# Performance work log

Measured on AMD Instinct MI355X. Metric: run time of the kernel, lower is better.

## Reference

```python
import jax, jax.numpy as jnp
import numpy as np

NEG_INF = -1e30
NUM_HEADS = 4
MEM_LEN = 16
RECURRENT_STEPS = 3
B, PLEN, GLEN, D = 16, 512, 16384, 256


def gated_attn(query, key, value, key_mask, Wq, Wk, Wv, Wo, Wg, bg):
    # GatedMultiHeadAttn.forward (pre/post lnorm off, add_zero_attn off, eval dropout)
    b, qlen, _ = query.shape
    klen = key.shape[1]
    hidden = Wq.shape[1]
    hd = hidden // NUM_HEADS
    hq = (query @ Wq).reshape(b, qlen, NUM_HEADS, hd)
    hk = (key @ Wk).reshape(b, klen, NUM_HEADS, hd)
    hv = (value @ Wv).reshape(b, klen, NUM_HEADS, hd)
    scale = 1.0 / np.sqrt(hd).astype(np.float32)
    score = jnp.einsum('bind,bjnd->bijn', hq, hk) * scale
    score = jnp.where((key_mask == 0)[:, None, :, None], NEG_INF, score)
    attn = jax.nn.softmax(score, axis=2)  # normalize over keys j
    vec = jnp.einsum('bijn,bjnd->bind', attn, hv).reshape(b, qlen, hidden)
    attn_out = vec @ Wo
    gate = jax.nn.sigmoid(jnp.concatenate([query, attn_out], axis=-1) @ Wg + bg)
    return gate * query + (1.0 - gate) * attn_out


def _attn_params(key, query_dim, kv_dim, hidden):
    ks = jax.random.split(key, 6)
    scale = 1.0 / np.sqrt(hidden // NUM_HEADS)
    Wq = jax.random.normal(ks[0], (query_dim, hidden), jnp.float32) * scale
    Wk = jax.random.normal(ks[1], (kv_dim, hidden), jnp.float32) * scale
    Wv = jax.random.normal(ks[2], (kv_dim, hidden), jnp.float32) * scale
    Wo = jax.random.normal(ks[3], (hidden, query_dim), jnp.float32) * scale
    Wg = jax.random.normal(ks[4], (2 * query_dim, query_dim), jnp.float32) * scale
    bg = jnp.ones((query_dim,), jnp.float32)
    return Wq, Wk, Wv, Wo, Wg, bg


def setup_inputs() -> dict:
    key = jax.random.key(0)
    ks = jax.random.split(key, 4)
    inp = {
        'pattern': jax.random.normal(ks[0], (B, PLEN, D), jnp.float32),
        'graph': jax.random.normal(ks[1], (B, GLEN, D), jnp.float32),
        'pattern_mask': jnp.ones((B, PLEN), jnp.int32),
        'graph_mask': jnp.ones((B, GLEN), jnp.int32),
    }
    p = _attn_params(ks[2], D, D, D)
    g = _attn_params(ks[3], D, D, D)
    for n, v in zip(['p_Wq', 'p_Wk', 'p_Wv', 'p_Wo', 'p_Wg', 'p_bg'], p):
        inp[n] = v
    for n, v in zip(['g_Wq', 'g_Wk', 'g_Wv', 'g_Wo', 'g_Wg', 'g_bg'], g):
        inp[n] = v
    return inp


def reference(pattern, graph, pattern_mask, graph_mask,
              p_Wq, p_Wk, p_Wv, p_Wo, p_Wg, p_bg,
              g_Wq, g_Wk, g_Wv, g_Wo, g_Wg, g_bg):
    b, glen, d = graph.shape
    stride = glen // MEM_LEN
    kernel = glen - (MEM_LEN - 1) * stride
    assert stride == kernel  # mem_len divides glen -> avg_pool1d == segment mean
    mem = graph.reshape(b, MEM_LEN, kernel, d).mean(axis=2)  # init_mem 'mean'
    mem_mask = graph_mask.reshape(b, MEM_LEN, kernel).max(axis=2)
    for _ in range(RECURRENT_STEPS):
        mem = gated_attn(mem, pattern, pattern, pattern_mask,
                         p_Wq, p_Wk, p_Wv, p_Wo, p_Wg, p_bg)
        mem = gated_attn(mem, graph, graph, graph_mask,
                         g_Wq, g_Wk, g_Wv, g_Wo, g_Wg, g_bg)
    return mem
```

## Files before the change

kernel.cpp:

```cpp
#include <hip/hip_runtime.h>
#include <stdint.h>

#define NH 4
#define HD 64
#define DM 256
#define BB 16
#define PLEN 512
#define GLEN 16384
#define ML 16
#define NCH_MAX 32

typedef __attribute__((ext_vector_type(8))) short bf16x8;
typedef __attribute__((ext_vector_type(4))) short s16x4;
typedef __attribute__((ext_vector_type(4))) float f32x4;
struct fl4 { float x, y, z, w; };

#define MFMA16(a, b, c) __builtin_amdgcn_mfma_f32_16x16x32_bf16((a), (b), (c), 0, 0, 0)

__device__ __forceinline__ float bf2f(short x) {
  union { unsigned u; float f; } v;
  v.u = ((unsigned)(unsigned short)x) << 16;
  return v.f;
}
__device__ __forceinline__ short f2bf(float x) {
  union { float f; unsigned u; } v;
  v.f = x;
  unsigned u = v.u;
  u += 0x7fffu + ((u >> 16) & 1u);
  return (short)(u >> 16);
}

__global__ void detect_dtype(const short* __restrict__ pattern, int* __restrict__ flag) {
  int t = threadIdx.x;
  int bad = 0;
  for (int i = t; i < 4096; i += 256) {
    float v = bf2f(pattern[2 * i]);
    if (!(fabsf(v) < 1e10f)) bad++;
  }
  __shared__ int cnt;
  if (t == 0) cnt = 0;
  __syncthreads();
  if (bad) atomicAdd(&cnt, bad);
  __syncthreads();
  if (t == 0) flag[0] = (cnt > 8) ? 1 : 0;
}

__global__ __launch_bounds__(256) void convert_sum(
    const void* __restrict__ src, short* __restrict__ dst,
    float* __restrict__ partials, const int* __restrict__ flag, int do_sum) {
  int isf = flag[0];
  int t = threadIdx.x;
  int r4 = t >> 6, c4 = (t & 63) * 4;
  size_t row0 = (size_t)blockIdx.x * 128;
  float s0 = 0.f, s1 = 0.f, s2 = 0.f, s3 = 0.f;
  if (isf) {
    const float* sf = (const float*)src;
    for (int it = 0; it < 32; it++) {
      size_t row = row0 + it * 4 + r4;
      fl4 v = *(const fl4*)(sf + row * DM + c4);
      s0 += v.x; s1 += v.y; s2 += v.z; s3 += v.w;
      s16x4 o;
      o[0] = f2bf(v.x); o[1] = f2bf(v.y); o[2] = f2bf(v.z); o[3] = f2bf(v.w);
      *(s16x4*)(dst + row * DM + c4) = o;
    }
  } else {
    const short* sb = (const short*)src;
    for (int it = 0; it < 32; it++) {
      size_t row = row0 + it * 4 + r4;
      s16x4 v = *(const s16x4*)(sb + row * DM + c4);
      s0 += bf2f(v[0]); s1 += bf2f(v[1]); s2 += bf2f(v[2]); s3 += bf2f(v[3]);
      *(s16x4*)(dst + row * DM + c4) = v;
    }
  }
  if (!do_sum) return;
  __shared__ float part[4][256];
  part[r4][c4] = s0;
  part[r4][c4 + 1] = s1;
  part[r4][c4 + 2] = s2;
  part[r4][c4 + 3] = s3;
  __syncthreads();
  partials[(size_t)blockIdx.x * 256 + t] =
      part[0][t] + part[1][t] + part[2][t] + part[3][t];
}

__global__ __launch_bounds__(256) void finalize_q0(
    const float* __restrict__ partials, const void* __restrict__ Wq,
    float* __restrict__ mem, short* __restrict__ hq, const int* __restrict__ flag) {
  int b = blockIdx.x >> 4, m = blockIdx.x & 15;
  int t = threadIdx.x;
  int isf = flag[0];
  int p0 = b * 128 + m * 8;
  float s = 0.f;
#pragma unroll
  for (int i = 0; i < 8; i++) s += partials[(size_t)(p0 + i) * 256 + t];
  float v = s * (1.0f / 1024.0f);
  __shared__ float memrow[256];
  memrow[t] = bf2f(f2bf(v));
  mem[((size_t)b * ML + m) * DM + t] = v;
  __syncthreads();
  float acc = 0.f;
  if (isf) {
    const float* wf = (const float*)Wq;
    for (int k = 0; k < 256; k++)
      acc += memrow[k] * bf2f(f2bf(wf[(size_t)k * 256 + t]));
  } else {
    const short* wsp = (const short*)Wq;
    for (int k = 0; k < 256; k++)
      acc += memrow[k] * bf2f(wsp[(size_t)k * 256 + t]);
  }
  hq[((size_t)b * ML + m) * DM + t] = f2bf(acc);
}

struct WTArgs {
  const void* src[10];
  short* dst[10];
  int rows[10];
};

__global__ void transpose_w(WTArgs a, const int* __restrict__ flag) {
  int mid = blockIdx.z;
  int K = a.rows[mid];
  int tk = blockIdx.x, tn = blockIdx.y;
  if (tk * 32 >= K) return;
  int isf = flag[0];
  __shared__ short tile[32][33];
  const short* src = (const short*)a.src[mid];
  const float* srcf = (const float*)a.src[mid];
  short* dst = a.dst[mid];
  int tx = threadIdx.x, ty = threadIdx.y;
  for (int i = 0; i < 32; i += 8) {
    size_t idx = (size_t)(tk * 32 + ty + i) * 256 + tn * 32 + tx;
    tile[ty + i][tx] = isf ? f2bf(srcf[idx]) : src[idx];
  }
  __syncthreads();
  for (int i = 0; i < 32; i += 8)
    dst[(size_t)(tn * 32 + ty + i) * K + tk * 32 + tx] = tile[tx][ty + i];
}

__global__ void conv_bias(const void* p_bg, const void* g_bg, short* out,
                          const int* __restrict__ flag) {
  int t = threadIdx.x;
  int isf = flag[0];
  out[t] = isf ? f2bf(((const float*)p_bg)[t]) : ((const short*)p_bg)[t];
  out[256 + t] = isf ? f2bf(((const float*)g_bg)[t]) : ((const short*)g_bg)[t];
}

__global__ __launch_bounds__(512, 2) void proj_kv(
    const short* __restrict__ X, const short* __restrict__ WkT,
    const short* __restrict__ WvT, short* __restrict__ Kout,
    short* __restrict__ Vt, int L) {
  __shared__ __align__(16) short Xs[128 * 32];
  __shared__ __align__(16) short Ws[256 * 32];
  const short* WT = blockIdx.y ? WvT : WkT;
  int row0 = blockIdx.x * 128;
  int t = threadIdx.x;
  int wave = t >> 6, lane = t & 63, quad = lane >> 4, l16 = lane & 15;
  int wrow = (wave >> 2) * 64, wcol = (wave & 3) * 64;
  int tr = t >> 2, tc = t & 3;
  f32x4 z = {0.f, 0.f, 0.f, 0.f};
  f32x4 acc[4][4];
#pragma unroll
  for (int i = 0; i < 4; i++)
#pragma unroll
    for (int j = 0; j < 4; j++) acc[i][j] = z;

  for (int kk = 0; kk < 8; kk++) {
    bf16x8 x0 = *(const bf16x8*)(X + (size_t)(row0 + tr) * DM + kk * 32 + tc * 8);
    bf16x8 w0 = *(const bf16x8*)(WT + (size_t)tr * DM + kk * 32 + tc * 8);
    bf16x8 w1 = *(const bf16x8*)(WT + (size_t)(tr + 128) * DM + kk * 32 + tc * 8);
    *(bf16x8*)(Xs + tr * 32 + tc * 8) = x0;
    *(bf16x8*)(Ws + tr * 32 + tc * 8) = w0;
    *(bf16x8*)(Ws + (tr + 128) * 32 + tc * 8) = w1;
    __syncthreads();
    bf16x8 af[4], bfr[4];
#pragma unroll
    for (int rt = 0; rt < 4; rt++)
      af[rt] = *(const bf16x8*)(Xs + (wrow + rt * 16 + l16) * 32 + quad * 8);
#pragma unroll
    for (int ct = 0; ct < 4; ct++)
      bfr[ct] = *(const bf16x8*)(Ws + (wcol + ct * 16 + l16) * 32 + quad * 8);
#pragma unroll
    for (int rt = 0; rt < 4; rt++)
#pragma unroll
      for (int ct = 0; ct < 4; ct++)
        acc[rt][ct] = MFMA16(af[rt], bfr[ct], acc[rt][ct]);
    __syncthreads();
  }
  if (blockIdx.y == 0) {
#pragma unroll
    for (int rt = 0; rt < 4; rt++)
#pragma unroll
      for (int ct = 0; ct < 4; ct++) {
        int col = wcol + ct * 16 + l16;
#pragma unroll
        for (int r = 0; r < 4; r++) {
          int row = row0 + wrow + rt * 16 + quad * 4 + r;
          Kout[(size_t)row * DM + col] = f2bf(acc[rt][ct][r]);
        }
      }
  } else {
#pragma unroll
    for (int rt = 0; rt < 4; rt++) {
      int gr = row0 + wrow + rt * 16 + quad * 4;
      int bb = gr / L, j = gr % L;
#pragma unroll
      for (int ct = 0; ct < 4; ct++) {
        int c = wcol + ct * 16 + l16;
        s16x4 pv;
#pragma unroll
        for (int r = 0; r < 4; r++) pv[r] = f2bf(acc[rt][ct][r]);
        *(s16x4*)(Vt + ((size_t)bb * DM + c) * L + j) = pv;
      }
    }
  }
}

__global__ __launch_bounds__(256, 4) void flash_partial(
    const short* __restrict__ hq, const short* __restrict__ Kb,
    const short* __restrict__ Vt, const int* __restrict__ mask,
    float* __restrict__ pm, float* __restrict__ pl, float* __restrict__ pO,
    int L, int NCH) {
  int ch = blockIdx.x, b = blockIdx.y;
  int C = L / NCH;
  int t = threadIdx.x, wave = t >> 6, lane = t & 63, quad = lane >> 4, l16 = lane & 15;
  __shared__ __align__(16) short Plds[4][512];
  short* myP = &Plds[wave][0];
  const short* qbase = hq + ((size_t)b * ML + l16) * DM + wave * HD;
  bf16x8 aq0 = *(const bf16x8*)(qbase + quad * 8);
  bf16x8 aq1 = *(const bf16x8*)(qbase + 32 + quad * 8);
  f32x4 z = {0.f, 0.f, 0.f, 0.f};
  float m_run[4], l_run[4];
  f32x4 O[4];
#pragma unroll
  for (int r = 0; r < 4; r++) { m_run[r] = -1e30f; l_run[r] = 0.f; }
#pragma unroll
  for (int d = 0; d < 4; d++) O[d] = z;
  int j0 = ch * C;
  const float L2E = 1.44269504f;
  for (int jt = 0; jt < C; jt += 32) {
    f32x4 S[2];
#pragma unroll
    for (int tt = 0; tt < 2; tt++) {
      int j = j0 + jt + tt * 16 + l16;
      const short* kb = Kb + ((size_t)b * L + j) * DM + wave * HD;
      bf16x8 b0 = *(const bf16x8*)(kb + quad * 8);
      bf16x8 b1 = *(const bf16x8*)(kb + 32 + quad * 8);
      f32x4 s = MFMA16(aq0, b0, z);
      s = MFMA16(aq1, b1, s);
      int mk = mask[(size_t)b * L + j];
#pragma unroll
      for (int r = 0; r < 4; r++)
        S[tt][r] = mk ? s[r] * 0.125f : -1e30f;
    }
    float p[2][4], alpha[4];
#pragma unroll
    for (int r = 0; r < 4; r++) {
      float v = fmaxf(S[0][r], S[1][r]);
      v = fmaxf(v, __shfl_xor(v, 1, 16));
      v = fmaxf(v, __shfl_xor(v, 2, 16));
      v = fmaxf(v, __shfl_xor(v, 4, 16));
      v = fmaxf(v, __shfl_xor(v, 8, 16));
      float nm = fmaxf(m_run[r], v);
      alpha[r] = exp2f((m_run[r] - nm) * L2E);
      m_run[r] = nm;
      p[0][r] = exp2f((S[0][r] - nm) * L2E);
      p[1][r] = exp2f((S[1][r] - nm) * L2E);
      float ps = p[0][r] + p[1][r];
      ps += __shfl_xor(ps, 1, 16);
      ps += __shfl_xor(ps, 2, 16);
      ps += __shfl_xor(ps, 4, 16);
      ps += __shfl_xor(ps, 8, 16);
      l_run[r] = l_run[r] * alpha[r] + ps;
    }
#pragma unroll
    for (int d = 0; d < 4; d++)
#pragma unroll
      for (int r = 0; r < 4; r++) O[d][r] *= alpha[r];
#pragma unroll
    for (int tt = 0; tt < 2; tt++)
#pragma unroll
      for (int r = 0; r < 4; r++)
        myP[(quad * 4 + r) * 32 + tt * 16 + l16] = f2bf(p[tt][r]);
    __syncthreads();
    bf16x8 ap = *(const bf16x8*)(myP + l16 * 32 + quad * 8);
#pragma unroll
    for (int d = 0; d < 4; d++) {
      const short* vb = Vt + ((size_t)b * DM + wave * HD + d * 16 + l16) * L + j0 + jt + quad * 8;
      bf16x8 bv = *(const bf16x8*)vb;
      O[d] = MFMA16(ap, bv, O[d]);
    }
    __syncthreads();
  }
  size_t base = (((size_t)b * NCH + ch) * NH + wave) * ML;
  if (l16 == 0) {
#pragma unroll
    for (int r = 0; r < 4; r++) {
      pm[base + quad * 4 + r] = m_run[r];
      pl[base + quad * 4 + r] = l_run[r];
    }
  }
#pragma unroll
  for (int d = 0; d < 4; d++)
#pragma unroll
    for (int r = 0; r < 4; r++)
      pO[(base + quad * 4 + r) * 64 + d * 16 + l16] = O[d][r];
}

__global__ __launch_bounds__(256, 2) void epilogue(
    const float* __restrict__ pm, const float* __restrict__ pl,
    const float* __restrict__ pO, int NCH,
    float* __restrict__ mem, const short* __restrict__ WoT,
    const short* __restrict__ WgT, const short* __restrict__ bg,
    const short* __restrict__ WqT, short* __restrict__ hq,
    void* __restrict__ outb, const int* __restrict__ flag) {
  int b = blockIdx.x, t = threadIdx.x;
  int isf = flag[0];
  __shared__ float w_lds[NCH_MAX * 64];
  __shared__ float invL[64];
  __shared__ __align__(16) short vec_bf[ML * DM];
  __shared__ __align__(16) short mem_bf[ML * DM];
  __shared__ __align__(16) short attn_bf[ML * DM];
  __shared__ float attn_f[ML * DM];
  __shared__ __align__(16) short memn_bf[ML * DM];

  for (int idx = t; idx < ML * DM; idx += 256)
    mem_bf[idx] = f2bf(mem[(size_t)b * ML * DM + idx]);
  if (t < 64) {
    size_t base = (size_t)b * NCH * NH * ML + t;
    float M = -1e30f;
    for (int ch = 0; ch < NCH; ch++)
      M = fmaxf(M, pm[base + (size_t)ch * NH * ML]);
    float Ls = 0.f;
    for (int ch = 0; ch < NCH; ch++) {
      float w = exp2f((pm[base + (size_t)ch * NH * ML] - M) * 1.44269504f);
      w_lds[ch * 64 + t] = w;
      Ls += w * pl[base + (size_t)ch * NH * ML];
    }
    invL[t] = 1.0f / Ls;
  }
  __syncthreads();
  {
    int n = t >> 6, d = t & 63;
    for (int i = 0; i < 16; i++) {
      size_t pb = ((size_t)b * NCH * NH * ML + n * ML + i) * 64 + d;
      float o = 0.f;
      for (int ch = 0; ch < NCH; ch++)
        o += w_lds[ch * 64 + n * 16 + i] * pO[pb + (size_t)ch * NH * ML * 64];
      vec_bf[i * DM + n * 64 + d] = f2bf(o * invL[n * 16 + i]);
    }
  }
  __syncthreads();
  int wave = t >> 6, lane = t & 63, quad = lane >> 4, l16 = lane & 15;
  f32x4 z = {0.f, 0.f, 0.f, 0.f};
  f32x4 acc[4];
#pragma unroll
  for (int c = 0; c < 4; c++) acc[c] = z;
#pragma unroll
  for (int kk = 0; kk < 8; kk++) {
    bf16x8 a = *(const bf16x8*)(vec_bf + l16 * DM + kk * 32 + quad * 8);
#pragma unroll
    for (int ct = 0; ct < 4; ct++) {
      const short* wb = WoT + (size_t)(wave * 64 + ct * 16 + l16) * DM + kk * 32 + quad * 8;
      acc[ct] = MFMA16(a, *(const bf16x8*)wb, acc[ct]);
    }
  }
#pragma unroll
  for (int ct = 0; ct < 4; ct++)
#pragma unroll
    for (int r = 0; r < 4; r++) {
      int row = quad * 4 + r, col = wave * 64 + ct * 16 + l16;
      attn_f[row * DM + col] = acc[ct][r];
      attn_bf[row * DM + col] = f2bf(acc[ct][r]);
    }
  __syncthreads();
  f32x4 g[4];
#pragma unroll
  for (int c = 0; c < 4; c++) g[c] = z;
#pragma unroll
  for (int kk = 0; kk < 16; kk++) {
    bf16x8 a = (kk < 8)
        ? *(const bf16x8*)(mem_bf + l16 * DM + kk * 32 + quad * 8)
        : *(const bf16x8*)(attn_bf + l16 * DM + (kk - 8) * 32 + quad * 8);
#pragma unroll
    for (int ct = 0; ct < 4; ct++) {
      const short* wb = WgT + (size_t)(wave * 64 + ct * 16 + l16) * 512 + kk * 32 + quad * 8;
      g[ct] = MFMA16(a, *(const bf16x8*)wb, g[ct]);
    }
  }
#pragma unroll
  for (int ct = 0; ct < 4; ct++)
#pragma unroll
    for (int r = 0; r < 4; r++) {
      int row = quad * 4 + r, col = wave * 64 + ct * 16 + l16;
      float x = g[ct][r] + bf2f(bg[col]);
      float gg = 1.0f / (1.0f + exp2f(-x * 1.44269504f));
      float old = mem[(size_t)b * ML * DM + row * DM + col];
      float mn = gg * old + (1.0f - gg) * attn_f[row * DM + col];
      mem[(size_t)b * ML * DM + row * DM + col] = mn;
      memn_bf[row * DM + col] = f2bf(mn);
      if (outb) {
        size_t oi = (size_t)b * ML * DM + row * DM + col;
        if (isf) ((float*)outb)[oi] = mn;
        else ((short*)outb)[oi] = f2bf(mn);
      }
    }
  __syncthreads();
  if (WqT) {
    f32x4 h[4];
#pragma unroll
    for (int c = 0; c < 4; c++) h[c] = z;
#pragma unroll
    for (int kk = 0; kk < 8; kk++) {
      bf16x8 a = *(const bf16x8*)(memn_bf + l16 * DM + kk * 32 + quad * 8);
#pragma unroll
      for (int ct = 0; ct < 4; ct++) {
        const short* wb = WqT + (size_t)(wave * 64 + ct * 16 + l16) * DM + kk * 32 + quad * 8;
        h[ct] = MFMA16(a, *(const bf16x8*)wb, h[ct]);
      }
    }
#pragma unroll
    for (int ct = 0; ct < 4; ct++)
#pragma unroll
      for (int r = 0; r < 4; r++)
        hq[(size_t)b * ML * DM + (quad * 4 + r) * DM + wave * 64 + ct * 16 + l16] = f2bf(h[ct][r]);
  }
}

extern "C" void kernel_launch(void* const* d_in, const int* in_sizes, int n_in,
                              void* d_out, int out_size, void* d_ws, size_t ws_size,
                              hipStream_t stream) {
  const void* pattern = d_in[0];
  const void* graph = d_in[1];
  const int* pmask = (const int*)d_in[2];
  const int* gmask = (const int*)d_in[3];

  char* ws = (char*)d_ws;
  size_t off = 0;
  auto alloc = [&](size_t bytes) {
    void* p = ws + off;
    off = (off + bytes + 255) & ~(size_t)255;
    return p;
  };
  int* flag = (int*)alloc(4);
  int rows[10] = {256, 256, 256, 256, 512, 256, 256, 256, 256, 512};
  int srcidx[10] = {4, 5, 6, 7, 8, 10, 11, 12, 13, 14};
  short* WT[10];
  for (int i = 0; i < 10; i++) WT[i] = (short*)alloc((size_t)rows[i] * 256 * 2);
  short* bgc = (short*)alloc(512 * 2);
  short* Kp = (short*)alloc((size_t)BB * PLEN * DM * 2);
  short* Vpt = (short*)alloc((size_t)BB * PLEN * DM * 2);
  short* Kg = (short*)alloc((size_t)BB * GLEN * DM * 2);
  short* Vgt = (short*)alloc((size_t)BB * GLEN * DM * 2);
  short* hq = (short*)alloc((size_t)BB * ML * DM * 2);
  float* memf = (float*)alloc((size_t)BB * ML * DM * 4);
  float* pm = (float*)alloc((size_t)BB * NCH_MAX * NH * ML * 4);
  float* pl = (float*)alloc((size_t)BB * NCH_MAX * NH * ML * 4);
  float* pO = (float*)alloc((size_t)BB * NCH_MAX * NH * ML * 64 * 4);
  float* partG = (float*)alloc((size_t)(BB * GLEN / 128) * 256 * 4);
  short* gbf = (short*)alloc((size_t)BB * GLEN * DM * 2);
  short* pbf = (short*)alloc((size_t)BB * PLEN * DM * 2);
  if (off > ws_size) return;

  detect_dtype<<<dim3(1), dim3(256), 0, stream>>>((const short*)pattern, flag);

  WTArgs wa;
  for (int i = 0; i < 10; i++) {
    wa.src[i] = d_in[srcidx[i]];
    wa.dst[i] = WT[i];
    wa.rows[i] = rows[i];
  }
  transpose_w<<<dim3(16, 8, 10), dim3(32, 8), 0, stream>>>(wa, flag);
  conv_bias<<<dim3(1), dim3(256), 0, stream>>>(d_in[9], d_in[15], bgc, flag);

  convert_sum<<<dim3(BB * GLEN / 128), dim3(256), 0, stream>>>(graph, gbf, partG, flag, 1);
  convert_sum<<<dim3(BB * PLEN / 128), dim3(256), 0, stream>>>(pattern, pbf, (float*)nullptr, flag, 0);
  finalize_q0<<<dim3(BB * ML), dim3(256), 0, stream>>>(partG, d_in[4], memf, hq, flag);

  proj_kv<<<dim3(BB * PLEN / 128, 2), dim3(512), 0, stream>>>(pbf, WT[1], WT[2], Kp, Vpt, PLEN);
  proj_kv<<<dim3(BB * GLEN / 128, 2), dim3(512), 0, stream>>>(gbf, WT[6], WT[7], Kg, Vgt, GLEN);

  for (int s = 0; s < 3; s++) {
    flash_partial<<<dim3(8, BB), dim3(256), 0, stream>>>(hq, Kp, Vpt, pmask, pm, pl, pO, PLEN, 8);
    epilogue<<<dim3(BB), dim3(256), 0, stream>>>(pm, pl, pO, 8, memf, WT[3], WT[4], bgc,
                                                 (const short*)WT[5], hq, (void*)nullptr, flag);
    bool last = (s == 2);
    flash_partial<<<dim3(32, BB), dim3(256), 0, stream>>>(hq, Kg, Vgt, gmask, pm, pl, pO, GLEN, 32);
    epilogue<<<dim3(BB), dim3(256), 0, stream>>>(pm, pl, pO, 32, memf, WT[8], WT[9], bgc + 256,
                                                 last ? (const short*)nullptr : (const short*)WT[0],
                                                 hq, last ? d_out : (void*)nullptr, flag);
  }
}
```

Baseline: 1.195 ms.

## Fuse input conversion and segment sums into K/V projection kernel

Replaces the separate convert_sum pass (fp32→bf16 copy plus column sums) and the two-pass proj_kv with one kernel. Each 64-row block loads the raw input once, converts it into a swizzled LDS tile holding the full K dimension, writes segment partial sums, and computes both K and V with split waves reading weights straight from global/L2. This removes the round trip of the bf16 graph copy through HBM and reading X twice, at the cost of larger LDS use and uncached weight reads per wave.

```diff
diff --git a/kernel.cpp b/kernel.cpp
--- a/kernel.cpp
+++ b/kernel.cpp
@@ -45,42 +45,108 @@
   if (t == 0) flag[0] = (cnt > 8) ? 1 : 0;
 }
 
-__global__ __launch_bounds__(256) void convert_sum(
-    const void* __restrict__ src, short* __restrict__ dst,
-    float* __restrict__ partials, const int* __restrict__ flag, int do_sum) {
-  int isf = flag[0];
-  int t = threadIdx.x;
-  int r4 = t >> 6, c4 = (t & 63) * 4;
-  size_t row0 = (size_t)blockIdx.x * 128;
-  float s0 = 0.f, s1 = 0.f, s2 = 0.f, s3 = 0.f;
+__global__ __launch_bounds__(512, 4) void proj_kv_fused(
+    const void* __restrict__ Xraw, const short* __restrict__ WkT,
+    const short* __restrict__ WvT, short* __restrict__ Kout,
+    short* __restrict__ Vt, int L, float* __restrict__ partials,
+    const int* __restrict__ flag) {
+  __shared__ __align__(16) short Xs[64 * DM];
+  __shared__ float scr[16 * DM];
+  const int isf = flag[0];
+  const int t = threadIdx.x;
+  const int row0 = blockIdx.x * 64;
+  const int tc2 = t & 31, tr2 = t >> 5;
+  float s[8];
+#pragma unroll
+  for (int j = 0; j < 8; j++) s[j] = 0.f;
   if (isf) {
-    const float* sf = (const float*)src;
-    for (int it = 0; it < 32; it++) {
-      size_t row = row0 + it * 4 + r4;
-      fl4 v = *(const fl4*)(sf + row * DM + c4);
-      s0 += v.x; s1 += v.y; s2 += v.z; s3 += v.w;
-      s16x4 o;
-      o[0] = f2bf(v.x); o[1] = f2bf(v.y); o[2] = f2bf(v.z); o[3] = f2bf(v.w);
-      *(s16x4*)(dst + row * DM + c4) = o;
+    const float* xf = (const float*)Xraw + (size_t)row0 * DM + tc2 * 8;
+#pragma unroll
+    for (int it = 0; it < 4; it++) {
+      int row = it * 16 + tr2;
+      fl4 v0 = *(const fl4*)(xf + (size_t)row * DM);
+      fl4 v1 = *(const fl4*)(xf + (size_t)row * DM + 4);
+      s[0] += v0.x; s[1] += v0.y; s[2] += v0.z; s[3] += v0.w;
+      s[4] += v1.x; s[5] += v1.y; s[6] += v1.z; s[7] += v1.w;
+      bf16x8 o;
+      o[0] = f2bf(v0.x); o[1] = f2bf(v0.y); o[2] = f2bf(v0.z); o[3] = f2bf(v0.w);
+      o[4] = f2bf(v1.x); o[5] = f2bf(v1.y); o[6] = f2bf(v1.z); o[7] = f2bf(v1.w);
+      *(bf16x8*)(Xs + row * DM + (tc2 ^ (row & 7)) * 8) = o;
     }
   } else {
-    const short* sb = (const short*)src;
-    for (int it = 0; it < 32; it++) {
-      size_t row = row0 + it * 4 + r4;
-      s16x4 v = *(const s16x4*)(sb + row * DM + c4);
-      s0 += bf2f(v[0]); s1 += bf2f(v[1]); s2 += bf2f(v[2]); s3 += bf2f(v[3]);
-      *(s16x4*)(dst + row * DM + c4) = v;
-    }
-  }
-  if (!do_sum) return;
-  __shared__ float part[4][256];
-  part[r4][c4] = s0;
-  part[r4][c4 + 1] = s1;
-  part[r4][c4 + 2] = s2;
-  part[r4][c4 + 3] = s3;
-  __syncthreads();
-  partials[(size_t)blockIdx.x * 256 + t] =
-      part[0][t] + part[1][t] + part[2][t] + part[3][t];
+    const short* xb = (const short*)Xraw + (size_t)row0 * DM + tc2 * 8;
+#pragma unroll
+    for (int it = 0; it < 4; it++) {
+      int row = it * 16 + tr2;
+      bf16x8 v = *(const bf16x8*)(xb + (size_t)row * DM);
+#pragma unroll
+      for (int j = 0; j < 8; j++) s[j] += bf2f(v[j]);
+      *(bf16x8*)(Xs + row * DM + (tc2 ^ (row & 7)) * 8) = v;
+    }
+  }
+  if (partials) {
+#pragma unroll
+    for (int j = 0; j < 8; j++) scr[tr2 * DM + tc2 * 8 + j] = s[j];
+  }
+  __syncthreads();
+  if (partials && t < DM) {
+    float a = 0.f;
+#pragma unroll
+    for (int i = 0; i < 16; i++) a += scr[i * DM + t];
+    partials[(size_t)blockIdx.x * DM + t] = a;
+  }
+  const int wave = t >> 6, lane = t & 63, quad = lane >> 4, l16 = lane & 15;
+  const int kv = wave >> 2;
+  const int wc = (wave & 3) * 64;
+  const short* WT = kv ? WvT : WkT;
+  f32x4 z = {0.f, 0.f, 0.f, 0.f};
+  f32x4 acc[4][4];
+#pragma unroll
+  for (int i = 0; i < 4; i++)
+#pragma unroll
+    for (int j = 0; j < 4; j++) acc[i][j] = z;
+#pragma unroll
+  for (int kk = 0; kk < 8; kk++) {
+    bf16x8 a[4], bw[4];
+#pragma unroll
+    for (int rt = 0; rt < 4; rt++) {
+      int rw = rt * 16 + l16;
+      a[rt] = *(const bf16x8*)(Xs + rw * DM + (((kk * 4 + quad) ^ (rw & 7)) * 8));
+    }
+#pragma unroll
+    for (int ct = 0; ct < 4; ct++)
+      bw[ct] = *(const bf16x8*)(WT + (size_t)(wc + ct * 16 + l16) * DM + kk * 32 + quad * 8);
+#pragma unroll
+    for (int rt = 0; rt < 4; rt++)
+#pragma unroll
+      for (int ct = 0; ct < 4; ct++)
+        acc[rt][ct] = MFMA16(a[rt], bw[ct], acc[rt][ct]);
+  }
+  if (kv == 0) {
+#pragma unroll
+    for (int rt = 0; rt < 4; rt++)
+#pragma unroll
+      for (int ct = 0; ct < 4; ct++) {
+        int col = wc + ct * 16 + l16;
+#pragma unroll
+        for (int r = 0; r < 4; r++)
+          Kout[(size_t)(row0 + rt * 16 + quad * 4 + r) * DM + col] = f2bf(acc[rt][ct][r]);
+      }
+  } else {
+    int bb = row0 / L, j0v = row0 % L;
+#pragma unroll
+    for (int rt = 0; rt < 4; rt++) {
+      int j = j0v + rt * 16 + quad * 4;
+#pragma unroll
+      for (int ct = 0; ct < 4; ct++) {
+        int c = wc + ct * 16 + l16;
+        s16x4 pv;
+#pragma unroll
+        for (int r = 0; r < 4; r++) pv[r] = f2bf(acc[rt][ct][r]);
+        *(s16x4*)(Vt + ((size_t)bb * DM + c) * L + j) = pv;
+      }
+    }
+  }
 }
 
 __global__ __launch_bounds__(256) void finalize_q0(
@@ -89,10 +155,10 @@
   int b = blockIdx.x >> 4, m = blockIdx.x & 15;
   int t = threadIdx.x;
   int isf = flag[0];
-  int p0 = b * 128 + m * 8;
+  int p0 = b * 256 + m * 16;
   float s = 0.f;
 #pragma unroll
-  for (int i = 0; i < 8; i++) s += partials[(size_t)(p0 + i) * 256 + t];
+  for (int i = 0; i < 16; i++) s += partials[(size_t)(p0 + i) * 256 + t];
   float v = s * (1.0f / 1024.0f);
   __shared__ float memrow[256];
   memrow[t] = bf2f(f2bf(v));
@@ -143,76 +209,6 @@
   int isf = flag[0];
   out[t] = isf ? f2bf(((const float*)p_bg)[t]) : ((const short*)p_bg)[t];
   out[256 + t] = isf ? f2bf(((const float*)g_bg)[t]) : ((const short*)g_bg)[t];
-}
-
-__global__ __launch_bounds__(512, 2) void proj_kv(
-    const short* __restrict__ X, const short* __restrict__ WkT,
-    const short* __restrict__ WvT, short* __restrict__ Kout,
-    short* __restrict__ Vt, int L) {
-  __shared__ __align__(16) short Xs[128 * 32];
-  __shared__ __align__(16) short Ws[256 * 32];
-  const short* WT = blockIdx.y ? WvT : WkT;
-  int row0 = blockIdx.x * 128;
-  int t = threadIdx.x;
-  int wave = t >> 6, lane = t & 63, quad = lane >> 4, l16 = lane & 15;
-  int wrow = (wave >> 2) * 64, wcol = (wave & 3) * 64;
-  int tr = t >> 2, tc = t & 3;
-  f32x4 z = {0.f, 0.f, 0.f, 0.f};
-  f32x4 acc[4][4];
-#pragma unroll
-  for (int i = 0; i < 4; i++)
-#pragma unroll
-    for (int j = 0; j < 4; j++) acc[i][j] = z;
-
-  for (int kk = 0; kk < 8; kk++) {
-    bf16x8 x0 = *(const bf16x8*)(X + (size_t)(row0 + tr) * DM + kk * 32 + tc * 8);
-    bf16x8 w0 = *(const bf16x8*)(WT + (size_t)tr * DM + kk * 32 + tc * 8);
-    bf16x8 w1 = *(const bf16x8*)(WT + (size_t)(tr + 128) * DM + kk * 32 + tc * 8);
-    *(bf16x8*)(Xs + tr * 32 + tc * 8) = x0;
-    *(bf16x8*)(Ws + tr * 32 + tc * 8) = w0;
-    *(bf16x8*)(Ws + (tr + 128) * 32 + tc * 8) = w1;
-    __syncthreads();
-    bf16x8 af[4], bfr[4];
-#pragma unroll
-    for (int rt = 0; rt < 4; rt++)
-      af[rt] = *(const bf16x8*)(Xs + (wrow + rt * 16 + l16) * 32 + quad * 8);
-#pragma unroll
-    for (int ct = 0; ct < 4; ct++)
-      bfr[ct] = *(const bf16x8*)(Ws + (wcol + ct * 16 + l16) * 32 + quad * 8);
-#pragma unroll
-    for (int rt = 0; rt < 4; rt++)
-#pragma unroll
-      for (int ct = 0; ct < 4; ct++)
-        acc[rt][ct] = MFMA16(af[rt], bfr[ct], acc[rt][ct]);
-    __syncthreads();
-  }
-  if (blockIdx.y == 0) {
-#pragma unroll
-    for (int rt = 0; rt < 4; rt++)
-#pragma unroll
-      for (int ct = 0; ct < 4; ct++) {
-        int col = wcol + ct * 16 + l16;
-#pragma unroll
-        for (int r = 0; r < 4; r++) {
-          int row = row0 + wrow + rt * 16 + quad * 4 + r;
-          Kout[(size_t)row * DM + col] = f2bf(acc[rt][ct][r]);
-        }
-      }
-  } else {
-#pragma unroll
-    for (int rt = 0; rt < 4; rt++) {
-      int gr = row0 + wrow + rt * 16 + quad * 4;
-      int bb = gr / L, j = gr % L;
-#pragma unroll
-      for (int ct = 0; ct < 4; ct++) {
-        int c = wcol + ct * 16 + l16;
-        s16x4 pv;
-#pragma unroll
-        for (int r = 0; r < 4; r++) pv[r] = f2bf(acc[rt][ct][r]);
-        *(s16x4*)(Vt + ((size_t)bb * DM + c) * L + j) = pv;
-      }
-    }
-  }
 }
 
 __global__ __launch_bounds__(256, 4) void flash_partial(
@@ -456,9 +452,7 @@
   float* pm = (float*)alloc((size_t)BB * NCH_MAX * NH * ML * 4);
   float* pl = (float*)alloc((size_t)BB * NCH_MAX * NH * ML * 4);
   float* pO = (float*)alloc((size_t)BB * NCH_MAX * NH * ML * 64 * 4);
-  float* partG = (float*)alloc((size_t)(BB * GLEN / 128) * 256 * 4);
-  short* gbf = (short*)alloc((size_t)BB * GLEN * DM * 2);
-  short* pbf = (short*)alloc((size_t)BB * PLEN * DM * 2);
+  float* partG = (float*)alloc((size_t)(BB * GLEN / 64) * 256 * 4);
   if (off > ws_size) return;
 
   detect_dtype<<<dim3(1), dim3(256), 0, stream>>>((const short*)pattern, flag);
@@ -472,12 +466,11 @@
   transpose_w<<<dim3(16, 8, 10), dim3(32, 8), 0, stream>>>(wa, flag);
   conv_bias<<<dim3(1), dim3(256), 0, stream>>>(d_in[9], d_in[15], bgc, flag);
 
-  convert_sum<<<dim3(BB * GLEN / 128), dim3(256), 0, stream>>>(graph, gbf, partG, flag, 1);
-  convert_sum<<<dim3(BB * PLEN / 128), dim3(256), 0, stream>>>(pattern, pbf, (float*)nullptr, flag, 0);
+  proj_kv_fused<<<dim3(BB * GLEN / 64), dim3(512), 0, stream>>>(
+      graph, WT[6], WT[7], Kg, Vgt, GLEN, partG, flag);
+  proj_kv_fused<<<dim3(BB * PLEN / 64), dim3(512), 0, stream>>>(
+      pattern, WT[1], WT[2], Kp, Vpt, PLEN, (float*)nullptr, flag);
   finalize_q0<<<dim3(BB * ML), dim3(256), 0, stream>>>(partG, d_in[4], memf, hq, flag);
-
-  proj_kv<<<dim3(BB * PLEN / 128, 2), dim3(512), 0, stream>>>(pbf, WT[1], WT[2], Kp, Vpt, PLEN);
-  proj_kv<<<dim3(BB * GLEN / 128, 2), dim3(512), 0, stream>>>(gbf, WT[6], WT[7], Kg, Vgt, GLEN);
 
   for (int s = 0; s < 3; s++) {
     flash_partial<<<dim3(8, BB), dim3(256), 0, stream>>>(hq, Kp, Vpt, pmask, pm, pl, pO, PLEN, 8);
```

Result: faster. 1.109 ms (-7.2%).
